# Kernel optimization log

Measured on AMD Instinct MI355X. Metric: run time of the kernel, lower is better.

## Reference

```python
import jax, jax.numpy as jnp
import numpy as np
from jax import lax

B, CIN, N = 4, 3, 2048
H, COUT, LEVELS = 128, 3, 3
HEADS = 8

# jnp.convolve(x, f, 'same') with len(f)=8 == correlation with f[::-1], x zero-padded (4,3).
# DWT then takes [::2], which is conv stride 2. IDWT zero-upsamples (lhs_dilation=2) then
# convolves 'same' with f[::-1], i.e. correlation with f, padding (4,4).

def _dwt(x, wlow, whigh):
    # x: (M, L) -> approx, detail each (M, L//2)
    rhs = jnp.stack([wlow[::-1], whigh[::-1]])[:, None, :]  # (2,1,8)
    out = lax.conv_general_dilated(x[:, None, :], rhs, window_strides=(2,),
                                   padding=[(4, 3)],
                                   dimension_numbers=('NCH', 'OIH', 'NCH'))
    return out[:, 0, :], out[:, 1, :]

def _idwt(a, d, wlow, whigh):
    # a, d: (M, L) -> (M, 2L); recon_low + recon_high fused as a 2-in-channel conv
    lhs = jnp.stack([a, d], axis=1)               # (M,2,L)
    rhs = jnp.stack([wlow, whigh])[None, :, :]    # (1,2,8)
    out = lax.conv_general_dilated(lhs, rhs, window_strides=(1,),
                                   padding=[(4, 4)], lhs_dilation=(2,),
                                   dimension_numbers=('NCH', 'OIH', 'NCH'))
    return out[:, 0, :]


def setup_inputs() -> dict:
    key = jax.random.key(0)
    ks = jax.random.split(key, 12)
    db4_low = jnp.array([0.23037781, 0.71484657, 0.63088076, -0.02798376,
                         -0.18703481, 0.03084138, 0.03288301, -0.0105974], jnp.float32)
    db4_high = jnp.array([-0.0105974, -0.03288301, 0.03084138, 0.18703481,
                          -0.02798376, -0.63088076, 0.71484657, -0.23037781], jnp.float32)
    def s(k, shape, fan_in):
        return jax.random.normal(k, shape, jnp.float32) * (1.0 / fan_in) ** 0.5
    return {
        'x': jax.random.normal(ks[0], (B, CIN, N), jnp.float32),
        'wlow': db4_low, 'whigh': db4_high,
        'Win': s(ks[1], (CIN, H), CIN), 'b_in': jnp.zeros((H,), jnp.float32),
        'W1': s(ks[2], (LEVELS, 2, 2 * H), 2), 'b1': jnp.zeros((LEVELS, 2 * H), jnp.float32),
        'W2': s(ks[3], (LEVELS, 2 * H, H), 2 * H), 'b2': jnp.zeros((LEVELS, H), jnp.float32),
        'Wq': s(ks[4], (H, H), H), 'bq': jnp.zeros((H,), jnp.float32),
        'Wk': s(ks[5], (H, H), H), 'bk': jnp.zeros((H,), jnp.float32),
        'Wv': s(ks[6], (H, H), H), 'bv': jnp.zeros((H,), jnp.float32),
        'Wo': s(ks[7], (H, H), H), 'bo': jnp.zeros((H,), jnp.float32),
        'Wout': s(ks[8], (H, COUT), H), 'bout': jnp.zeros((COUT,), jnp.float32),
    }


def reference(x, wlow, whigh, Win, b_in, W1, b1, W2, b2,
              Wq, bq, Wk, bk, Wv, bv, Wo, bo, Wout, bout):
    Bx = x.shape[0]
    # input projection: (B,CIN,N) -> (B,H,N)
    xp = jnp.einsum('bcn,ch->bhn', x, Win) + b_in[None, :, None]
    cur = xp.reshape(Bx * H, N)  # per-(batch,channel) 1D signals, fully batched
    proc = []  # processed coeffs per level; note approx == detail after the shared mean
    for lvl in range(LEVELS):
        a, d = _dwt(cur, wlow, whigh)                 # (M, L)
        c = jnp.stack([a, d], axis=-1)                # (M, L, 2)
        h = jax.nn.gelu(c @ W1[lvl] + b1[lvl])        # (M, L, 2H)
        p = (h @ W2[lvl] + b2[lvl]).mean(axis=-1)     # (M, L): mean over hidden dim
        proc.append(p)
        cur = a
    rec = proc[-1]  # start from deepest processed approx
    for lvl in range(LEVELS - 1, -1, -1):
        rec = _idwt(rec, proc[lvl], wlow, whigh)
    y = rec.reshape(Bx, H, N)
    # cross-level attention: standard MHA with embed_dim=H, 8 heads, no dropout
    seq = y.transpose(0, 2, 1)  # (B,N,H)
    dh = H // HEADS
    q = (seq @ Wq + bq).reshape(Bx, N, HEADS, dh)
    k = (seq @ Wk + bk).reshape(Bx, N, HEADS, dh)
    v = (seq @ Wv + bv).reshape(Bx, N, HEADS, dh)
    att = jnp.einsum('bqhd,bkhd->bhqk', q, k) * (dh ** -0.5)
    att = jax.nn.softmax(att, axis=-1)
    o = jnp.einsum('bhqk,bkhd->bqhd', att, v).reshape(Bx, N, H)
    o = o @ Wo + bo
    out = o @ Wout + bout  # (B,N,COUT)
    return out.transpose(0, 2, 1)  # (B,COUT,N)
```

## Files before the change

### kernel.cpp

```cpp
#include <hip/hip_runtime.h>

#define N_    2048
#define H_    128
#define B_    4
#define CIN_  3
#define COUT_ 3
#define LOG2E 1.44269504089f

__device__ __forceinline__ float gelu_tanh(float x) {
    float x2 = x * x;
    float e = __builtin_amdgcn_exp2f(x * fmaf(-0.10294340397f, x2, -2.30220899f));
    return x * __builtin_amdgcn_rcpf(1.0f + e);
}

__global__ void prep_kernel(const float* __restrict__ W1, const float* __restrict__ b1,
                            const float* __restrict__ W2, const float* __restrict__ b2,
                            const float* __restrict__ Wo, const float* __restrict__ bo,
                            const float* __restrict__ Wout, const float* __restrict__ bout,
                            float4* __restrict__ wpack, float* __restrict__ b2m,
                            float* __restrict__ wf, float* __restrict__ bf) {
    int gid = blockIdx.x * 256 + threadIdx.x;
    if (gid < 768) {
        const float* r = W2 + (size_t)gid * 128;
        float s = 0.f;
        for (int h = 0; h < 128; ++h) s += r[h];
        int lvl = gid >> 8, k = gid & 255;
        wpack[gid] = make_float4(W1[lvl * 512 + k], W1[lvl * 512 + 256 + k],
                                 b1[gid], s * (1.0f / 128.0f));
    } else if (gid < 771) {
        int lvl = gid - 768;
        const float* r = b2 + lvl * 128;
        float s = 0.f;
        for (int h = 0; h < 128; ++h) s += r[h];
        b2m[lvl] = s * (1.0f / 128.0f);
    } else if (gid >= 1024 && gid < 1408) {
        int e = gid - 1024;
        int h = e / 3, c = e - 3 * h;
        float s = 0.f;
        for (int j = 0; j < 128; ++j) s = fmaf(Wo[h * 128 + j], Wout[j * 3 + c], s);
        wf[e] = s;
    } else if (gid >= 1408 && gid < 1411) {
        int c = gid - 1408;
        float s = bout[c];
        for (int j = 0; j < 128; ++j) s = fmaf(bo[j], Wout[j * 3 + c], s);
        bf[c] = s;
    }
}

__global__ __launch_bounds__(256) void wavelet_fused_kernel(
        const float* __restrict__ x, const float* __restrict__ Win,
        const float* __restrict__ b_in,
        const float* __restrict__ wlow, const float* __restrict__ whigh,
        const float4* __restrict__ wpack, const float* __restrict__ b2m,
        float* __restrict__ r0g) {
    __shared__ float cur[2048];
    __shared__ float aA[1024];
    __shared__ float pp0[1024];
    __shared__ float aB[512];
    __shared__ float pp1[512];
    __shared__ float pp2[256];
    __shared__ float r2s[512];
    __shared__ float r1s[1024];
    int tid = threadIdx.x;
    int m = blockIdx.x;
    int b = m >> 7, h = m & 127;
    float w0 = Win[h], w1 = Win[128 + h], w2 = Win[256 + h];
    float bi = b_in[h];
    float wl[8], wh[8];
#pragma unroll
    for (int t = 0; t < 8; ++t) { wl[t] = wlow[t]; wh[t] = whigh[t]; }

    const float* xr = x + (size_t)b * (CIN_ * N_);
    for (int idx = tid; idx < 2048; idx += 256) {
        float v = bi;
        v = fmaf(xr[idx], w0, v);
        v = fmaf(xr[N_ + idx], w1, v);
        v = fmaf(xr[2 * N_ + idx], w2, v);
        cur[idx] = v;
    }
    __syncthreads();

    {
        float a4[4], d4[4], acc4[4];
#pragma unroll
        for (int u = 0; u < 4; ++u) {
            int i = tid + u * 256;
            int j0 = 2 * i - 4;
            float a = 0.f, d = 0.f;
#pragma unroll
            for (int t = 0; t < 8; ++t) {
                int j = j0 + t;
                float xv = ((unsigned)j < 2048u) ? cur[j] : 0.f;
                a = fmaf(xv, wl[7 - t], a);
                d = fmaf(xv, wh[7 - t], d);
            }
            a4[u] = a; d4[u] = d; aA[i] = a; acc4[u] = 0.f;
        }
#pragma unroll 4
        for (int kk = 0; kk < 256; ++kk) {
            float4 w = wpack[kk];
#pragma unroll
            for (int u = 0; u < 4; ++u) {
                float t = fmaf(a4[u], w.x, fmaf(d4[u], w.y, w.z));
                acc4[u] = fmaf(gelu_tanh(t), w.w, acc4[u]);
            }
        }
        float bb = b2m[0];
#pragma unroll
        for (int u = 0; u < 4; ++u) pp0[tid + u * 256] = acc4[u] + bb;
    }
    __syncthreads();

    {
        float a2v[2], d2v[2], acc2[2];
#pragma unroll
        for (int u = 0; u < 2; ++u) {
            int i = tid + u * 256;
            int j0 = 2 * i - 4;
            float a = 0.f, d = 0.f;
#pragma unroll
            for (int t = 0; t < 8; ++t) {
                int j = j0 + t;
                float xv = ((unsigned)j < 1024u) ? aA[j] : 0.f;
                a = fmaf(xv, wl[7 - t], a);
                d = fmaf(xv, wh[7 - t], d);
            }
            a2v[u] = a; d2v[u] = d; aB[i] = a; acc2[u] = 0.f;
        }
#pragma unroll 4
        for (int kk = 0; kk < 256; ++kk) {
            float4 w = wpack[256 + kk];
#pragma unroll
            for (int u = 0; u < 2; ++u) {
                float t = fmaf(a2v[u], w.x, fmaf(d2v[u], w.y, w.z));
                acc2[u] = fmaf(gelu_tanh(t), w.w, acc2[u]);
            }
        }
        float bb = b2m[1];
#pragma unroll
        for (int u = 0; u < 2; ++u) pp1[tid + u * 256] = acc2[u] + bb;
    }
    __syncthreads();

    {
        int j0 = 2 * tid - 4;
        float a = 0.f, d = 0.f;
#pragma unroll
        for (int t = 0; t < 8; ++t) {
            int j = j0 + t;
            float xv = ((unsigned)j < 512u) ? aB[j] : 0.f;
            a = fmaf(xv, wl[7 - t], a);
            d = fmaf(xv, wh[7 - t], d);
        }
        float acc = 0.f;
#pragma unroll 4
        for (int kk = 0; kk < 256; ++kk) {
            float4 w = wpack[512 + kk];
            float t = fmaf(a, w.x, fmaf(d, w.y, w.z));
            acc = fmaf(gelu_tanh(t), w.w, acc);
        }
        pp2[tid] = acc + b2m[2];
    }
    __syncthreads();

#pragma unroll
    for (int u = 0; u < 2; ++u) {
        int ii = tid + u * 256;
        int podd = ii & 1;
        int off0 = (ii >> 1) - 2 + podd;
        float r = 0.f;
#pragma unroll
        for (int s = 0; s < 4; ++s) {
            int idx = off0 + s;
            float av = ((unsigned)idx < 256u) ? pp2[idx] : 0.f;
            r = fmaf(av, wl[2 * s + podd] + wh[2 * s + podd], r);
        }
        r2s[ii] = r;
    }
    __syncthreads();

#pragma unroll
    for (int u = 0; u < 4; ++u) {
        int ii = tid + u * 256;
        int podd = ii & 1;
        int off0 = (ii >> 1) - 2 + podd;
        float r = 0.f;
#pragma unroll
        for (int s = 0; s < 4; ++s) {
            int idx = off0 + s;
            bool ok = (unsigned)idx < 512u;
            float av = ok ? r2s[idx] : 0.f;
            float dv = ok ? pp1[idx] : 0.f;
            r = fmaf(av, wl[2 * s + podd], r);
            r = fmaf(dv, wh[2 * s + podd], r);
        }
        r1s[ii] = r;
    }
    __syncthreads();

    float* orow = r0g + (size_t)m * 2048;
#pragma unroll
    for (int u = 0; u < 8; ++u) {
        int ii = tid + u * 256;
        int podd = ii & 1;
        int off0 = (ii >> 1) - 2 + podd;
        float r = 0.f;
#pragma unroll
        for (int s = 0; s < 4; ++s) {
            int idx = off0 + s;
            bool ok = (unsigned)idx < 1024u;
            float av = ok ? r1s[idx] : 0.f;
            float dv = ok ? pp0[idx] : 0.f;
            r = fmaf(av, wl[2 * s + podd], r);
            r = fmaf(dv, wh[2 * s + podd], r);
        }
        orow[ii] = r;
    }
}

__global__ __launch_bounds__(384) void qkv_kernel(
        const float* __restrict__ r0,
        const float* __restrict__ Wq, const float* __restrict__ bq,
        const float* __restrict__ Wk, const float* __restrict__ bk,
        const float* __restrict__ Wv, const float* __restrict__ bv,
        float* __restrict__ qB, float* __restrict__ kB, float* __restrict__ vB) {
    int tid = threadIdx.x;
    int rowbase = blockIdx.x * 16;
    int b  = rowbase >> 11;
    int n0 = rowbase & 2047;

    const float* W; const float* bias; float* dst; int jj;
    if (tid < 128)      { W = Wq; bias = bq; dst = qB; jj = tid; }
    else if (tid < 256) { W = Wk; bias = bk; dst = kB; jj = tid - 128; }
    else                { W = Wv; bias = bv; dst = vB; jj = tid - 256; }

    const float* abase = r0 + (size_t)b * (H_ * N_) + n0;
    float acc[16];
#pragma unroll
    for (int r = 0; r < 16; ++r) acc[r] = 0.f;
    for (int h = 0; h < 128; ++h) {
        float w = W[h * 128 + jj];
        const float* ar = abase + (size_t)h * N_;
#pragma unroll
        for (int r = 0; r < 16; ++r) acc[r] = fmaf(ar[r], w, acc[r]);
    }
    float bb = bias[jj];
    int head = jj >> 4, t = jj & 15;
    size_t obase = ((size_t)(b * 8 + head) * N_) * 16 + t;
#pragma unroll
    for (int r = 0; r < 16; ++r)
        dst[obase + (size_t)(n0 + r) * 16] = acc[r] + bb;
}

#define DOT4(acc, qq, aa) do { acc = fmaf(qq.x, aa.x, acc); acc = fmaf(qq.y, aa.y, acc); \
                               acc = fmaf(qq.z, aa.z, acc); acc = fmaf(qq.w, aa.w, acc); } while (0)
#define SCALE4(oo, c)     do { oo.x *= c; oo.y *= c; oo.z *= c; oo.w *= c; } while (0)
#define AXPY4(oo, p, aa)  do { oo.x = fmaf(p, aa.x, oo.x); oo.y = fmaf(p, aa.y, oo.y); \
                               oo.z = fmaf(p, aa.z, oo.z); oo.w = fmaf(p, aa.w, oo.w); } while (0)

template<int KS>
__global__ __launch_bounds__(64, 3) void attn_kernel(
        const float* __restrict__ qb, const float* __restrict__ kb,
        const float* __restrict__ vb,
        float* __restrict__ part_o, float* __restrict__ part_ml) {
    int lane  = threadIdx.x;
    int blk   = blockIdx.x;
    int split = blk % KS;
    int qblk  = (blk / KS) & 15;
    int bh    = blk / (16 * KS);
    int nA    = qblk * 128 + lane;
    int nB    = nA + 64;

    const float sc = 0.25f * LOG2E;
    const float4* qra = (const float4*)(qb + ((size_t)bh * N_ + nA) * 16);
    const float4* qrb = (const float4*)(qb + ((size_t)bh * N_ + nB) * 16);
    float4 qa0 = qra[0], qa1 = qra[1], qa2 = qra[2], qa3 = qra[3];
    float4 qb0 = qrb[0], qb1 = qrb[1], qb2 = qrb[2], qb3 = qrb[3];
    SCALE4(qa0, sc); SCALE4(qa1, sc); SCALE4(qa2, sc); SCALE4(qa3, sc);
    SCALE4(qb0, sc); SCALE4(qb1, sc); SCALE4(qb2, sc); SCALE4(qb3, sc);

    float mA = -3.0e38f, lA = 0.f, mB = -3.0e38f, lB = 0.f;
    float4 oA0 = {0,0,0,0}, oA1 = oA0, oA2 = oA0, oA3 = oA0;
    float4 oB0 = oA0, oB1 = oA0, oB2 = oA0, oB3 = oA0;

    const float* kbase = kb + (size_t)bh * (N_ * 16);
    const float* vbase = vb + (size_t)bh * (N_ * 16);
    int k0 = split * (N_ / KS);
#pragma unroll 2
    for (int t = k0; t < k0 + N_ / KS; ++t) {
        const float4* kr = (const float4*)(kbase + (size_t)t * 16);
        float4 k0v = kr[0], k1v = kr[1], k2v = kr[2], k3v = kr[3];
        float sA0 = 0.f, sA1 = 0.f, sB0 = 0.f, sB1 = 0.f;
        DOT4(sA0, qa0, k0v); DOT4(sA1, qa1, k1v); DOT4(sA0, qa2, k2v); DOT4(sA1, qa3, k3v);
        DOT4(sB0, qb0, k0v); DOT4(sB1, qb1, k1v); DOT4(sB0, qb2, k2v); DOT4(sB1, qb3, k3v);
        float sA = sA0 + sA1, sB = sB0 + sB1;
        if (__any((sA > mA + 8.f) || (sB > mB + 8.f))) {
            float mnA = fmaxf(mA, sA), mnB = fmaxf(mB, sB);
            float cA = __builtin_amdgcn_exp2f(mA - mnA);
            float cB = __builtin_amdgcn_exp2f(mB - mnB);
            lA *= cA; lB *= cB;
            SCALE4(oA0, cA); SCALE4(oA1, cA); SCALE4(oA2, cA); SCALE4(oA3, cA);
            SCALE4(oB0, cB); SCALE4(oB1, cB); SCALE4(oB2, cB); SCALE4(oB3, cB);
            mA = mnA; mB = mnB;
        }
        float pA = __builtin_amdgcn_exp2f(sA - mA);
        float pB = __builtin_amdgcn_exp2f(sB - mB);
        lA += pA; lB += pB;
        const float4* vr = (const float4*)(vbase + (size_t)t * 16);
        float4 v0 = vr[0], v1 = vr[1], v2 = vr[2], v3 = vr[3];
        AXPY4(oA0, pA, v0); AXPY4(oA1, pA, v1); AXPY4(oA2, pA, v2); AXPY4(oA3, pA, v3);
        AXPY4(oB0, pB, v0); AXPY4(oB1, pB, v1); AXPY4(oB2, pB, v2); AXPY4(oB3, pB, v3);
    }

    int qgA = bh * N_ + nA, qgB = bh * N_ + nB;
    float4* poA = (float4*)part_o + ((size_t)split * 65536 + qgA) * 4;
    poA[0] = oA0; poA[1] = oA1; poA[2] = oA2; poA[3] = oA3;
    float4* poB = (float4*)part_o + ((size_t)split * 65536 + qgB) * 4;
    poB[0] = oB0; poB[1] = oB1; poB[2] = oB2; poB[3] = oB3;
    ((float2*)part_ml)[(size_t)split * 65536 + qgA] = make_float2(mA, lA);
    ((float2*)part_ml)[(size_t)split * 65536 + qgB] = make_float2(mB, lB);
}

template<int KS>
__global__ __launch_bounds__(512) void combine_final_kernel(
        const float* __restrict__ part_o, const float* __restrict__ part_ml,
        const float* __restrict__ wf, const float* __restrict__ bf,
        float* __restrict__ out) {
    __shared__ float ysh[64 * 129];
    int tid = threadIdx.x;
    int b = blockIdx.x >> 5, nb = blockIdx.x & 31;
    int head = tid >> 6, nl = tid & 63;
    int n = nb * 64 + nl;
    int qg = (b * 8 + head) * N_ + n;

    float m[KS], l[KS];
    float M = -3.0e38f;
#pragma unroll
    for (int s = 0; s < KS; ++s) {
        float2 ml = ((const float2*)part_ml)[(size_t)s * 65536 + qg];
        m[s] = ml.x; l[s] = ml.y;
        M = fmaxf(M, m[s]);
    }
    float w[KS], lt = 0.f;
#pragma unroll
    for (int s = 0; s < KS; ++s) {
        w[s] = __builtin_amdgcn_exp2f(m[s] - M);
        lt = fmaf(l[s], w[s], lt);
    }
    float inv = __builtin_amdgcn_rcpf(lt);
    float o[16];
#pragma unroll
    for (int j = 0; j < 16; ++j) o[j] = 0.f;
#pragma unroll
    for (int s = 0; s < KS; ++s) {
        const float4* po = (const float4*)part_o + ((size_t)s * 65536 + qg) * 4;
#pragma unroll
        for (int r = 0; r < 4; ++r) {
            float4 v = po[r];
            o[4*r+0] = fmaf(v.x, w[s], o[4*r+0]);
            o[4*r+1] = fmaf(v.y, w[s], o[4*r+1]);
            o[4*r+2] = fmaf(v.z, w[s], o[4*r+2]);
            o[4*r+3] = fmaf(v.w, w[s], o[4*r+3]);
        }
    }
    int col = head * 16;
#pragma unroll
    for (int j = 0; j < 16; ++j) ysh[nl * 129 + col + j] = o[j] * inv;
    __syncthreads();
    if (tid < 192) {
        int c = tid >> 6, nl2 = tid & 63;
        float acc = bf[c];
        const float* yr = ysh + nl2 * 129;
#pragma unroll 4
        for (int h = 0; h < 128; ++h) acc = fmaf(yr[h], wf[h * 3 + c], acc);
        out[((size_t)b * 3 + c) * N_ + nb * 64 + nl2] = acc;
    }
}

extern "C" void kernel_launch(void* const* d_in, const int* in_sizes, int n_in,
                              void* d_out, int out_size, void* d_ws, size_t ws_size,
                              hipStream_t stream) {
    const float* x    = (const float*)d_in[0];
    const float* wlow = (const float*)d_in[1];
    const float* whigh= (const float*)d_in[2];
    const float* Win  = (const float*)d_in[3];
    const float* b_in = (const float*)d_in[4];
    const float* W1   = (const float*)d_in[5];
    const float* b1   = (const float*)d_in[6];
    const float* W2   = (const float*)d_in[7];
    const float* b2   = (const float*)d_in[8];
    const float* Wq   = (const float*)d_in[9];
    const float* bq   = (const float*)d_in[10];
    const float* Wk   = (const float*)d_in[11];
    const float* bk   = (const float*)d_in[12];
    const float* Wv   = (const float*)d_in[13];
    const float* bv   = (const float*)d_in[14];
    const float* Wo   = (const float*)d_in[15];
    const float* bo   = (const float*)d_in[16];
    const float* Wout = (const float*)d_in[17];
    const float* bout = (const float*)d_in[18];
    float* out = (float*)d_out;
    (void)in_sizes; (void)n_in; (void)out_size;

    float* ws = (float*)d_ws;
    float* qBuf  = ws;
    float* kBuf  = ws + 1048576;
    float* vBuf  = ws + 2097152;
    float* base2 = ws + 3145728;
    float* r0    = base2;

    const size_t need8 = (3145728ull + 8ull * 1048576 + 8ull * 131072 + 4096ull) * 4;
    int KS = (ws_size >= need8) ? 8 : 4;

    float* part_o  = base2;
    float* part_ml = base2 + (size_t)KS * 1048576;
    float* smalls  = part_ml + (size_t)KS * 131072;
    float4* wpack = (float4*)smalls;
    float* b2m = smalls + 3072;
    float* wf  = smalls + 3088;
    float* bf  = smalls + 3472;

    prep_kernel<<<8, 256, 0, stream>>>(W1, b1, W2, b2, Wo, bo, Wout, bout, wpack, b2m, wf, bf);

    wavelet_fused_kernel<<<512, 256, 0, stream>>>(x, Win, b_in, wlow, whigh,
                                                  wpack, b2m, r0);

    qkv_kernel<<<512, 384, 0, stream>>>(r0, Wq, bq, Wk, bk, Wv, bv, qBuf, kBuf, vBuf);

    if (KS == 8) {
        attn_kernel<8><<<32 * 16 * 8, 64, 0, stream>>>(qBuf, kBuf, vBuf, part_o, part_ml);
        combine_final_kernel<8><<<128, 512, 0, stream>>>(part_o, part_ml, wf, bf, out);
    } else {
        attn_kernel<4><<<32 * 16 * 4, 64, 0, stream>>>(qBuf, kBuf, vBuf, part_o, part_ml);
        combine_final_kernel<4><<<128, 512, 0, stream>>>(part_o, part_ml, wf, bf, out);
    }
}
```

Before: 395.6 us.

## Stage K/V tiles in LDS, process four queries per thread, add 16-way split

```diff
diff --git a/kernel.cpp b/kernel.cpp
--- a/kernel.cpp
+++ b/kernel.cpp
@@ -259,78 +259,109 @@
                                oo.z = fmaf(p, aa.z, oo.z); oo.w = fmaf(p, aa.w, oo.w); } while (0)
 
 template<int KS>
-__global__ __launch_bounds__(64, 3) void attn_kernel(
+__global__ __launch_bounds__(128, 4) void attn_kernel(
         const float* __restrict__ qb, const float* __restrict__ kb,
         const float* __restrict__ vb,
         float* __restrict__ part_o, float* __restrict__ part_ml) {
-    int lane  = threadIdx.x;
+    __shared__ float4 kt4[512];
+    __shared__ float4 vt4[512];
+    int tid   = threadIdx.x;
     int blk   = blockIdx.x;
     int split = blk % KS;
-    int qblk  = (blk / KS) & 15;
-    int bh    = blk / (16 * KS);
-    int nA    = qblk * 128 + lane;
-    int nB    = nA + 64;
-
+    int qblk  = (blk / KS) & 3;
+    int bh    = blk / (4 * KS);
+
+    const float4* ksrc = (const float4*)(kb + (size_t)bh * (N_ * 16));
+    const float4* vsrc = (const float4*)(vb + (size_t)bh * (N_ * 16));
     const float sc = 0.25f * LOG2E;
-    const float4* qra = (const float4*)(qb + ((size_t)bh * N_ + nA) * 16);
-    const float4* qrb = (const float4*)(qb + ((size_t)bh * N_ + nB) * 16);
-    float4 qa0 = qra[0], qa1 = qra[1], qa2 = qra[2], qa3 = qra[3];
-    float4 qb0 = qrb[0], qb1 = qrb[1], qb2 = qrb[2], qb3 = qrb[3];
-    SCALE4(qa0, sc); SCALE4(qa1, sc); SCALE4(qa2, sc); SCALE4(qa3, sc);
-    SCALE4(qb0, sc); SCALE4(qb1, sc); SCALE4(qb2, sc); SCALE4(qb3, sc);
-
-    float mA = -3.0e38f, lA = 0.f, mB = -3.0e38f, lB = 0.f;
-    float4 oA0 = {0,0,0,0}, oA1 = oA0, oA2 = oA0, oA3 = oA0;
-    float4 oB0 = oA0, oB1 = oA0, oB2 = oA0, oB3 = oA0;
-
-    const float* kbase = kb + (size_t)bh * (N_ * 16);
-    const float* vbase = vb + (size_t)bh * (N_ * 16);
+
+    float4 q[4][4];
+    float  m[4], l[4];
+    float4 o[4][4];
+#pragma unroll
+    for (int qi = 0; qi < 4; ++qi) {
+        const float4* qr = (const float4*)(qb + ((size_t)bh * N_ + qblk * 512 + qi * 128 + tid) * 16);
+#pragma unroll
+        for (int j = 0; j < 4; ++j) { q[qi][j] = qr[j]; SCALE4(q[qi][j], sc); }
+        m[qi] = -3.0e38f; l[qi] = 0.f;
+#pragma unroll
+        for (int j = 0; j < 4; ++j) o[qi][j] = make_float4(0.f, 0.f, 0.f, 0.f);
+    }
+
     int k0 = split * (N_ / KS);
-#pragma unroll 2
-    for (int t = k0; t < k0 + N_ / KS; ++t) {
-        const float4* kr = (const float4*)(kbase + (size_t)t * 16);
-        float4 k0v = kr[0], k1v = kr[1], k2v = kr[2], k3v = kr[3];
-        float sA0 = 0.f, sA1 = 0.f, sB0 = 0.f, sB1 = 0.f;
-        DOT4(sA0, qa0, k0v); DOT4(sA1, qa1, k1v); DOT4(sA0, qa2, k2v); DOT4(sA1, qa3, k3v);
-        DOT4(sB0, qb0, k0v); DOT4(sB1, qb1, k1v); DOT4(sB0, qb2, k2v); DOT4(sB1, qb3, k3v);
-        float sA = sA0 + sA1, sB = sB0 + sB1;
-        if (__any((sA > mA + 8.f) || (sB > mB + 8.f))) {
-            float mnA = fmaxf(mA, sA), mnB = fmaxf(mB, sB);
-            float cA = __builtin_amdgcn_exp2f(mA - mnA);
-            float cB = __builtin_amdgcn_exp2f(mB - mnB);
-            lA *= cA; lB *= cB;
-            SCALE4(oA0, cA); SCALE4(oA1, cA); SCALE4(oA2, cA); SCALE4(oA3, cA);
-            SCALE4(oB0, cB); SCALE4(oB1, cB); SCALE4(oB2, cB); SCALE4(oB3, cB);
-            mA = mnA; mB = mnB;
-        }
-        float pA = __builtin_amdgcn_exp2f(sA - mA);
-        float pB = __builtin_amdgcn_exp2f(sB - mB);
-        lA += pA; lB += pB;
-        const float4* vr = (const float4*)(vbase + (size_t)t * 16);
-        float4 v0 = vr[0], v1 = vr[1], v2 = vr[2], v3 = vr[3];
-        AXPY4(oA0, pA, v0); AXPY4(oA1, pA, v1); AXPY4(oA2, pA, v2); AXPY4(oA3, pA, v3);
-        AXPY4(oB0, pB, v0); AXPY4(oB1, pB, v1); AXPY4(oB2, pB, v2); AXPY4(oB3, pB, v3);
-    }
-
-    int qgA = bh * N_ + nA, qgB = bh * N_ + nB;
-    float4* poA = (float4*)part_o + ((size_t)split * 65536 + qgA) * 4;
-    poA[0] = oA0; poA[1] = oA1; poA[2] = oA2; poA[3] = oA3;
-    float4* poB = (float4*)part_o + ((size_t)split * 65536 + qgB) * 4;
-    poB[0] = oB0; poB[1] = oB1; poB[2] = oB2; poB[3] = oB3;
-    ((float2*)part_ml)[(size_t)split * 65536 + qgA] = make_float2(mA, lA);
-    ((float2*)part_ml)[(size_t)split * 65536 + qgB] = make_float2(mB, lB);
+    for (int t0 = k0; t0 < k0 + N_ / KS; t0 += 128) {
+        __syncthreads();
+        const float4* ks = ksrc + t0 * 4;
+        const float4* vs = vsrc + t0 * 4;
+#pragma unroll
+        for (int u = 0; u < 4; ++u) {
+            kt4[tid + u * 128] = ks[tid + u * 128];
+            vt4[tid + u * 128] = vs[tid + u * 128];
+        }
+        __syncthreads();
+
+        for (int c0 = 0; c0 < 128; c0 += 4) {
+            float sv[4][4];
+            float cm[4] = {-3.0e38f, -3.0e38f, -3.0e38f, -3.0e38f};
+#pragma unroll
+            for (int c = 0; c < 4; ++c) {
+                int kr = (c0 + c) * 4;
+                float4 k0v = kt4[kr], k1v = kt4[kr+1], k2v = kt4[kr+2], k3v = kt4[kr+3];
+#pragma unroll
+                for (int qi = 0; qi < 4; ++qi) {
+                    float s0 = 0.f, s1 = 0.f;
+                    DOT4(s0, q[qi][0], k0v); DOT4(s1, q[qi][1], k1v);
+                    DOT4(s0, q[qi][2], k2v); DOT4(s1, q[qi][3], k3v);
+                    sv[qi][c] = s0 + s1;
+                    cm[qi] = fmaxf(cm[qi], sv[qi][c]);
+                }
+            }
+            bool need = (cm[0] > m[0] + 8.f) || (cm[1] > m[1] + 8.f) ||
+                        (cm[2] > m[2] + 8.f) || (cm[3] > m[3] + 8.f);
+            if (__any(need)) {
+#pragma unroll
+                for (int qi = 0; qi < 4; ++qi) {
+                    float mn = fmaxf(m[qi], cm[qi]);
+                    float cr = __builtin_amdgcn_exp2f(m[qi] - mn);
+                    l[qi] *= cr;
+#pragma unroll
+                    for (int j = 0; j < 4; ++j) SCALE4(o[qi][j], cr);
+                    m[qi] = mn;
+                }
+            }
+#pragma unroll
+            for (int c = 0; c < 4; ++c) {
+                int vr = (c0 + c) * 4;
+                float4 v0 = vt4[vr], v1 = vt4[vr+1], v2 = vt4[vr+2], v3 = vt4[vr+3];
+#pragma unroll
+                for (int qi = 0; qi < 4; ++qi) {
+                    float p = __builtin_amdgcn_exp2f(sv[qi][c] - m[qi]);
+                    l[qi] += p;
+                    AXPY4(o[qi][0], p, v0); AXPY4(o[qi][1], p, v1);
+                    AXPY4(o[qi][2], p, v2); AXPY4(o[qi][3], p, v3);
+                }
+            }
+        }
+    }
+#pragma unroll
+    for (int qi = 0; qi < 4; ++qi) {
+        int qg = bh * N_ + qblk * 512 + qi * 128 + tid;
+        float4* po = (float4*)part_o + ((size_t)split * 65536 + qg) * 4;
+        po[0] = o[qi][0]; po[1] = o[qi][1]; po[2] = o[qi][2]; po[3] = o[qi][3];
+        ((float2*)part_ml)[(size_t)split * 65536 + qg] = make_float2(m[qi], l[qi]);
+    }
 }
 
 template<int KS>
-__global__ __launch_bounds__(512) void combine_final_kernel(
+__global__ __launch_bounds__(256) void combine_final_kernel(
         const float* __restrict__ part_o, const float* __restrict__ part_ml,
         const float* __restrict__ wf, const float* __restrict__ bf,
         float* __restrict__ out) {
-    __shared__ float ysh[64 * 129];
+    __shared__ float ysh[32 * 129];
     int tid = threadIdx.x;
-    int b = blockIdx.x >> 5, nb = blockIdx.x & 31;
-    int head = tid >> 6, nl = tid & 63;
-    int n = nb * 64 + nl;
+    int b = blockIdx.x >> 6, nb = blockIdx.x & 63;
+    int head = tid >> 5, nl = tid & 31;
+    int n = nb * 32 + nl;
     int qg = (b * 8 + head) * N_ + n;
 
     float m[KS], l[KS];
@@ -367,13 +398,13 @@
 #pragma unroll
     for (int j = 0; j < 16; ++j) ysh[nl * 129 + col + j] = o[j] * inv;
     __syncthreads();
-    if (tid < 192) {
-        int c = tid >> 6, nl2 = tid & 63;
+    if (tid < 96) {
+        int c = tid >> 5, nl2 = tid & 31;
         float acc = bf[c];
         const float* yr = ysh + nl2 * 129;
 #pragma unroll 4
         for (int h = 0; h < 128; ++h) acc = fmaf(yr[h], wf[h * 3 + c], acc);
-        out[((size_t)b * 3 + c) * N_ + nb * 64 + nl2] = acc;
+        out[((size_t)b * 3 + c) * N_ + nb * 32 + nl2] = acc;
     }
 }
 
@@ -409,8 +440,9 @@
     float* base2 = ws + 3145728;
     float* r0    = base2;
 
-    const size_t need8 = (3145728ull + 8ull * 1048576 + 8ull * 131072 + 4096ull) * 4;
-    int KS = (ws_size >= need8) ? 8 : 4;
+    const size_t need16 = (3145728ull + 16ull * 1048576 + 16ull * 131072 + 4096ull) * 4;
+    const size_t need8  = (3145728ull +  8ull * 1048576 +  8ull * 131072 + 4096ull) * 4;
+    int KS = (ws_size >= need16) ? 16 : ((ws_size >= need8) ? 8 : 4);
 
     float* part_o  = base2;
     float* part_ml = base2 + (size_t)KS * 1048576;
@@ -427,11 +459,14 @@
 
     qkv_kernel<<<512, 384, 0, stream>>>(r0, Wq, bq, Wk, bk, Wv, bv, qBuf, kBuf, vBuf);
 
-    if (KS == 8) {
-        attn_kernel<8><<<32 * 16 * 8, 64, 0, stream>>>(qBuf, kBuf, vBuf, part_o, part_ml);
-        combine_final_kernel<8><<<128, 512, 0, stream>>>(part_o, part_ml, wf, bf, out);
+    if (KS == 16) {
+        attn_kernel<16><<<32 * 4 * 16, 128, 0, stream>>>(qBuf, kBuf, vBuf, part_o, part_ml);
+        combine_final_kernel<16><<<256, 256, 0, stream>>>(part_o, part_ml, wf, bf, out);
+    } else if (KS == 8) {
+        attn_kernel<8><<<32 * 4 * 8, 128, 0, stream>>>(qBuf, kBuf, vBuf, part_o, part_ml);
+        combine_final_kernel<8><<<256, 256, 0, stream>>>(part_o, part_ml, wf, bf, out);
     } else {
-        attn_kernel<4><<<32 * 16 * 4, 64, 0, stream>>>(qBuf, kBuf, vBuf, part_o, part_ml);
-        combine_final_kernel<4><<<128, 512, 0, stream>>>(part_o, part_ml, wf, bf, out);
-    }
-}
+        attn_kernel<4><<<32 * 4 * 4, 128, 0, stream>>>(qBuf, kBuf, vBuf, part_o, part_ml);
+        combine_final_kernel<4><<<256, 256, 0, stream>>>(part_o, part_ml, wf, bf, out);
+    }
+}
```

Result: slower. 1.178 ms (+197.9%).
